# Kernel tuning notes

Measured on AMD Instinct MI355X. Metric: run time of the kernel, lower is better.

Reference implementation:

```python
import jax, jax.numpy as jnp
import numpy as np

B, N, DX, E, H, HD, KH, FF = 8, 8192, 2, 128, 8, 16, 32, 128
G1, G2, PMAX = 32, 32, 32


def _ln(x, g, b):
    mu = jnp.mean(x, axis=-1, keepdims=True)
    var = jnp.mean((x - mu) ** 2, axis=-1, keepdims=True)
    return (x - mu) * jax.lax.rsqrt(var + 1e-5) * g + b


def _cumcount_row(idx):
    # for each element, number of earlier elements with the same value (stable)
    n = idx.shape[0]
    order = jnp.argsort(idx)  # stable
    si = idx[order]
    ar = jnp.arange(n)
    is_start = jnp.concatenate([jnp.ones((1,), bool), si[1:] != si[:-1]])
    seg_start = jax.lax.associative_scan(jnp.maximum, jnp.where(is_start, ar, 0))
    return jnp.zeros(n, jnp.int32).at[order].set((ar - seg_start).astype(jnp.int32))


def _forward(x, z, latent, Wq, Wk, Wv, Wo, bo, kW1, kb1, kW2, kb2,
             lnq_g, lnq_b, lnk_g, lnk_b, ln2_g, ln2_b, fW1, fb1, fW2, fb2,
             grid_n1, grid_n2, max_patch, num_heads):
    Bb, Nn, dx = x.shape
    e = latent.shape[0]
    dims = (grid_n1, grid_n2)
    M = grid_n1 * grid_n2
    P = max_patch
    h = num_heads
    hd = Wq.shape[1] // h
    # grid range from data (margin = 0), regular grid via linspace
    mins = [jnp.min(x[:, :, i]) for i in range(dx)]
    maxs = [jnp.max(x[:, :, i]) for i in range(dx)]
    axes = [jnp.linspace(mins[i], maxs[i], dims[i]) for i in range(dx)]
    x_grid = jnp.stack(jnp.meshgrid(*axes, indexing="ij"), axis=-1)  # [G1,G2,dx]
    x_grid_flat = x_grid.reshape(M, dx)
    # nearest grid cell per point: regular grid -> per-dim rounding
    flat = None
    for i in range(dx):
        step = (maxs[i] - mins[i]) / (dims[i] - 1)
        ii = jnp.clip(jnp.round((x[..., i] - mins[i]) / step), 0, dims[i] - 1).astype(jnp.int32)
        flat = ii if flat is None else flat * dims[i] + ii
    cell = flat  # [B,N]
    cumc = jax.vmap(_cumcount_row)(cell)          # slot within cell
    slot = jnp.where(cumc < P, cumc, P)           # overflow -> dummy slot (dropped)
    bidx = jnp.broadcast_to(jnp.arange(Bb)[:, None], (Bb, Nn))
    # scatter points into per-cell padded neighbour sets [B, M, P, d]
    jx = jnp.zeros((Bb, M, P + 1, dx), x.dtype).at[bidx, cell, slot].set(x)[:, :, :P]
    jz = jnp.zeros((Bb, M, P + 1, e), z.dtype).at[bidx, cell, slot].set(z)[:, :, :P]
    msk = jnp.zeros((Bb, M, P + 1), bool).at[bidx, cell, slot].set(True)[:, :, :P]
    xg = jnp.broadcast_to(x_grid_flat[None], (Bb, M, dx))
    zg = jnp.broadcast_to(latent[None, None, :], (Bb, M, e))
    # concatenate_x_grid=True: grid token prepended, always attended
    joint_x = jnp.concatenate([xg[:, :, None, :], jx], axis=2).reshape(Bb * M, P + 1, dx)
    joint_z = jnp.concatenate([zg[:, :, None, :], jz], axis=2).reshape(Bb * M, P + 1, e)
    att_mask = jnp.concatenate([jnp.ones((Bb, M, 1), bool), msk], axis=2).reshape(Bb * M, P + 1)
    xq = xg.reshape(Bb * M, 1, dx)
    zq = zg.reshape(Bb * M, 1, e)
    T = Bb * M
    # masked translation-equivariant cross-attention (pre-norm layer)
    q = jnp.einsum("tqe,ef->tqf", _ln(zq, lnq_g, lnq_b), Wq).reshape(T, 1, h, hd)
    zk_n = _ln(joint_z, lnk_g, lnk_b)
    k = jnp.einsum("tke,ef->tkf", zk_n, Wk).reshape(T, P + 1, h, hd)
    v = jnp.einsum("tke,ef->tkf", zk_n, Wv).reshape(T, P + 1, h, hd)
    dots = jnp.einsum("tqhd,tkhd->thqk", q, k) / jnp.sqrt(jnp.asarray(hd, q.dtype))
    diff = joint_x[:, None, :, :] - xq[:, :, None, :]            # [T,1,P+1,dx]
    kb = jnp.maximum(diff @ kW1 + kb1, 0.0) @ kW2 + kb2          # kernel bias [T,1,P+1,h]
    dots = dots + jnp.transpose(kb, (0, 3, 1, 2))
    dots = jnp.where(att_mask[:, None, None, :], dots, -1e9)
    A = jax.nn.softmax(dots, axis=-1)                            # [T,h,1,P+1]
    out = jnp.einsum("thqk,tkhd->tqhd", A, v).reshape(T, 1, h * hd)
    z_new = zq + out @ Wo + bo
    z_new = z_new + (jnp.maximum(_ln(z_new, ln2_g, ln2_b) @ fW1 + fb1, 0.0) @ fW2 + fb2)
    x_new = jnp.einsum("tqk,tkd->tqd", jnp.mean(A, axis=1), joint_x)  # TE location update
    x_grid_out = x_new.reshape(Bb, grid_n1, grid_n2, dx)
    z_grid_out = z_new.reshape(Bb, grid_n1, grid_n2, e)
    return (x_grid_out, z_grid_out)


def setup_inputs():
    key = jax.random.key(0)
    ks = jax.random.split(key, 12)
    s = 0.05
    return {
        "x": jax.random.uniform(ks[0], (B, N, DX), jnp.float32),
        "z": jax.random.normal(ks[1], (B, N, E), jnp.float32),
        "grid_n1": G1, "grid_n2": G2, "max_patch": PMAX, "num_heads": H,
        "latent": jax.random.normal(ks[2], (E,), jnp.float32),
        "Wq": jax.random.normal(ks[3], (E, H * HD), jnp.float32) * s,
        "Wk": jax.random.normal(ks[4], (E, H * HD), jnp.float32) * s,
        "Wv": jax.random.normal(ks[5], (E, H * HD), jnp.float32) * s,
        "Wo": jax.random.normal(ks[6], (H * HD, E), jnp.float32) * s,
        "bo": jnp.zeros((E,), jnp.float32),
        "kW1": jax.random.normal(ks[7], (DX, KH), jnp.float32) * s,
        "kb1": jnp.zeros((KH,), jnp.float32),
        "kW2": jax.random.normal(ks[8], (KH, H), jnp.float32) * s,
        "kb2": jnp.zeros((H,), jnp.float32),
        "lnq_g": jnp.ones((E,), jnp.float32), "lnq_b": jnp.zeros((E,), jnp.float32),
        "lnk_g": jnp.ones((E,), jnp.float32), "lnk_b": jnp.zeros((E,), jnp.float32),
        "ln2_g": jnp.ones((E,), jnp.float32), "ln2_b": jnp.zeros((E,), jnp.float32),
        "fW1": jax.random.normal(ks[9], (E, FF), jnp.float32) * s,
        "fb1": jnp.zeros((FF,), jnp.float32),
        "fW2": jax.random.normal(ks[10], (FF, E), jnp.float32) * s,
        "fb2": jnp.zeros((E,), jnp.float32),
    }


def reference(x, z, grid_n1, grid_n2, max_patch, num_heads, latent, Wq, Wk, Wv, Wo, bo,
              kW1, kb1, kW2, kb2, lnq_g, lnq_b, lnk_g, lnk_b, ln2_g, ln2_b,
              fW1, fb1, fW2, fb2):
    return _forward(x, z, latent, Wq, Wk, Wv, Wo, bo, kW1, kb1, kW2, kb2,
                    lnq_g, lnq_b, lnk_g, lnk_b, ln2_g, ln2_b, fW1, fb1, fW2, fb2,
                    grid_n1, grid_n2, max_patch, num_heads)
```

## Files before the change

kernel.cpp:

```cpp
#include <hip/hip_runtime.h>
#include <stdint.h>

#define NB 8
#define NN 8192
#define NE 128
#define NH 8
#define NHD 16
#define NKH 32
#define NFF 128
#define NG 32
#define NM 1024
#define NP 32
#define NT 8192
#define NPTS 65536

typedef __attribute__((ext_vector_type(8))) short bf16x8_t;
typedef __attribute__((ext_vector_type(4))) float f32x4_t;

#define WS_MM      0
#define WS_D0      64
#define WS_Q       128
#define WS_VG      640
#define WS_PART    1152
#define WS_CNT     2048
#define WS_CELL    34816
#define WS_PIDX    296960
#define WS_WVT     1345536
#define WS_WOT     1411072
#define WS_FW1T    1443840
#define WS_FW2T    1476608
#define WS_WKQT    1509376
#define WS_SCORES  1513472
#define WS_KV      4194304

__device__ __forceinline__ unsigned short f2bf(float f) {
    unsigned u = __float_as_uint(f);
    u += 0x7FFFu + ((u >> 16) & 1u);
    return (unsigned short)(u >> 16);
}
__device__ __forceinline__ float bflo(unsigned w) { return __uint_as_float(w << 16); }
__device__ __forceinline__ float bfhi(unsigned w) { return __uint_as_float(w & 0xFFFF0000u); }

__global__ __launch_bounds__(256) void k_setup(
        const float* __restrict__ x,
        const float* __restrict__ Wk, const float* __restrict__ Wv, const float* __restrict__ Wo,
        const float* __restrict__ fW1, const float* __restrict__ fW2,
        const float* __restrict__ latent, const float* __restrict__ Wq,
        const float* __restrict__ lnq_g, const float* __restrict__ lnq_b,
        const float* __restrict__ lnk_g, const float* __restrict__ lnk_b,
        const float* __restrict__ kb1, const float* __restrict__ kW2, const float* __restrict__ kb2,
        int* __restrict__ cnt,
        unsigned short* __restrict__ WvT, unsigned short* __restrict__ WoT,
        unsigned short* __restrict__ fW1T, unsigned short* __restrict__ fW2T,
        float* __restrict__ ws_q, float* __restrict__ ws_vg, float* __restrict__ ws_d0,
        unsigned short* __restrict__ WkqT,
        float4* __restrict__ part) {
    int blk = blockIdx.x;
    int t = threadIdx.x;
    if (blk < 16) {
        __shared__ float s_t[64][65];
        const float* src; unsigned short* dst;
        int n0, k0;
        if (blk < 4) {
            int tn = blk >> 1, tk = blk & 1;
            n0 = tn * 64; k0 = tk * 64;
            src = Wv; dst = WvT;
        } else {
            int m = (blk - 4) >> 2, s4 = (blk - 4) & 3;
            int tn = s4 >> 1, tk = s4 & 1;
            n0 = tn * 64; k0 = tk * 64;
            src = (m == 0) ? Wo : (m == 1) ? fW1 : fW2;
            dst = (m == 0) ? WoT : (m == 1) ? fW1T : fW2T;
        }
        int tx = t & 63, ty = t >> 6;
        #pragma unroll
        for (int r = 0; r < 16; ++r) {
            int kr = r * 4 + ty;
            s_t[kr][tx] = src[(k0 + kr) * 128 + n0 + tx];
        }
        __syncthreads();
        #pragma unroll
        for (int r = 0; r < 16; ++r) {
            int nr = r * 4 + ty;
            dst[(n0 + nr) * 128 + k0 + tx] = f2bf(s_t[tx][nr]);
        }
    } else if (blk < 48) {
        int idx = (blk - 16) * 256 + t;
        cnt[idx] = 0;
    } else if (blk == 48) {
        __shared__ float s_qn[128], s_kn[128], s_q[128], s_kg[128];
        __shared__ float s_mu, s_rstd;
        if (t < 64) {
            float v0 = latent[t], v1 = latent[t + 64];
            float s = v0 + v1;
            for (int m = 32; m > 0; m >>= 1) s += __shfl_xor(s, m);
            float mu = s * (1.0f / 128.0f);
            float d0 = v0 - mu, d1 = v1 - mu;
            float q = d0 * d0 + d1 * d1;
            for (int m = 32; m > 0; m >>= 1) q += __shfl_xor(q, m);
            if (t == 0) { s_mu = mu; s_rstd = rsqrtf(q * (1.0f / 128.0f) + 1e-5f); }
        }
        __syncthreads();
        if (t < 128) {
            float nv = (latent[t] - s_mu) * s_rstd;
            s_qn[t] = nv * lnq_g[t] + lnq_b[t];
            s_kn[t] = nv * lnk_g[t] + lnk_b[t];
        }
        __syncthreads();
        if (t < 128) {
            float aq = 0.f, ak = 0.f, av = 0.f;
            for (int e = 0; e < 128; ++e) {
                aq += s_qn[e] * Wq[e * 128 + t];
                ak += s_kn[e] * Wk[e * 128 + t];
                av += s_kn[e] * Wv[e * 128 + t];
            }
            s_q[t] = aq; s_kg[t] = ak;
            ws_q[t] = aq; ws_vg[t] = av;
        }
        __syncthreads();
        if (t < 128) {
            const float* wr = Wk + t * 128;
            #pragma unroll
            for (int h = 0; h < 8; ++h) {
                float a = 0.f;
                #pragma unroll
                for (int d = 0; d < 16; ++d) a += wr[h * 16 + d] * s_q[h * 16 + d];
                WkqT[h * 128 + t] = f2bf(a * 0.25f);
                WkqT[(h + 8) * 128 + t] = 0;
            }
        }
        if (t < 8) {
            float acc = 0.f;
            for (int d = 0; d < 16; ++d) acc += s_q[t * 16 + d] * s_kg[t * 16 + d];
            float kb0 = kb2[t];
            for (int j = 0; j < 32; ++j) kb0 += fmaxf(kb1[j], 0.f) * kW2[j * 8 + t];
            ws_d0[t] = acc * 0.25f + kb0;
        }
    } else {
        __shared__ float s_red[4][4];
        int pb = blk - 49;
        const float4* xp = (const float4*)x + pb * 1024;
        float mn0 = 1e30f, mx0 = -1e30f, mn1 = 1e30f, mx1 = -1e30f;
        #pragma unroll
        for (int it = 0; it < 4; ++it) {
            float4 v = xp[it * 256 + t];
            mn0 = fminf(mn0, fminf(v.x, v.z)); mx0 = fmaxf(mx0, fmaxf(v.x, v.z));
            mn1 = fminf(mn1, fminf(v.y, v.w)); mx1 = fmaxf(mx1, fmaxf(v.y, v.w));
        }
        #pragma unroll
        for (int m = 32; m > 0; m >>= 1) {
            mn0 = fminf(mn0, __shfl_xor(mn0, m)); mx0 = fmaxf(mx0, __shfl_xor(mx0, m));
            mn1 = fminf(mn1, __shfl_xor(mn1, m)); mx1 = fmaxf(mx1, __shfl_xor(mx1, m));
        }
        int w = t >> 6;
        if ((t & 63) == 0) {
            s_red[w][0] = mn0; s_red[w][1] = mn1; s_red[w][2] = mx0; s_red[w][3] = mx1;
        }
        __syncthreads();
        if (t == 0) {
            float a0 = fminf(fminf(s_red[0][0], s_red[1][0]), fminf(s_red[2][0], s_red[3][0]));
            float a1 = fminf(fminf(s_red[0][1], s_red[1][1]), fminf(s_red[2][1], s_red[3][1]));
            float b0 = fmaxf(fmaxf(s_red[0][2], s_red[1][2]), fmaxf(s_red[2][2], s_red[3][2]));
            float b1 = fmaxf(fmaxf(s_red[0][3], s_red[1][3]), fmaxf(s_red[2][3], s_red[3][3]));
            part[pb] = make_float4(a0, a1, b0, b1);
        }
    }
}

__global__ __launch_bounds__(256) void k_binkv(
        const float* __restrict__ x, const float* __restrict__ z,
        const float4* __restrict__ part, float* __restrict__ mm,
        const float* __restrict__ lnk_g, const float* __restrict__ lnk_b,
        const unsigned short* __restrict__ WkqT,
        const float* __restrict__ kW1, const float* __restrict__ kb1,
        const float* __restrict__ kW2, const float* __restrict__ kb2,
        const unsigned short* __restrict__ WvT, unsigned short* __restrict__ kv,
        float* __restrict__ scores,
        int* __restrict__ cell, int* __restrict__ cnt, int* __restrict__ ptIdx) {
    int t = threadIdx.x;
    if (blockIdx.x >= 1024) {
        int l = t & 63;
        float mn0 = 1e30f, mn1 = 1e30f, mx0 = -1e30f, mx1 = -1e30f;
        if (l < 32) { float4 p = part[l]; mn0 = p.x; mn1 = p.y; mx0 = p.z; mx1 = p.w; }
        #pragma unroll
        for (int m = 32; m > 0; m >>= 1) {
            mn0 = fminf(mn0, __shfl_xor(mn0, m)); mx0 = fmaxf(mx0, __shfl_xor(mx0, m));
            mn1 = fminf(mn1, __shfl_xor(mn1, m)); mx1 = fmaxf(mx1, __shfl_xor(mx1, m));
        }
        if (blockIdx.x == 1024 && t == 0) {
            mm[0] = mn0; mm[1] = mn1; mm[2] = mx0; mm[3] = mx1;
        }
        int i = (blockIdx.x - 1024) * 256 + t;
        float st0 = (mx0 - mn0) / 31.0f, st1 = (mx1 - mn1) / 31.0f;
        float2 xv = ((const float2*)x)[i];
        int i0 = (int)rintf((xv.x - mn0) / st0); i0 = min(max(i0, 0), 31);
        int i1 = (int)rintf((xv.y - mn1) / st1); i1 = min(max(i1, 0), 31);
        int c = i0 * 32 + i1;
        cell[i] = c;
        int bb = i >> 13;
        int slot = atomicAdd(&cnt[bb * NM + c], 1);
        if (slot < NP) ptIdx[(bb * NM + c) * NP + slot] = i & (NN - 1);
        return;
    }
    __shared__ unsigned short s_zn[64][136];
    __shared__ unsigned short s_stage[4][16][68];
    int w = t >> 6, lane = t & 63;
    long base = (long)blockIdx.x * 64;
    int sub = lane >> 5;
    int lq = lane & 31;
    int mrow = lane & 15, quad = lane >> 4;

    float mn0 = 1e30f, mn1 = 1e30f, mx0 = -1e30f, mx1 = -1e30f;
    if (lane < 32) { float4 p = part[lane]; mn0 = p.x; mn1 = p.y; mx0 = p.z; mx1 = p.w; }
    #pragma unroll
    for (int m = 32; m > 0; m >>= 1) {
        mn0 = fminf(mn0, __shfl_xor(mn0, m)); mx0 = fmaxf(mx0, __shfl_xor(mx0, m));
        mn1 = fminf(mn1, __shfl_xor(mn1, m)); mx1 = fmaxf(mx1, __shfl_xor(mx1, m));
    }
    int ptl = w * 16 + mrow;
    float2 xv2 = ((const float2*)x)[base + ptl];

    int th = w >> 1, fh = w & 1;
    bf16x8_t afrag[4][4];
    #pragma unroll
    for (int j = 0; j < 4; ++j) {
        const unsigned short* ap = WvT + ((fh * 4 + j) * 16 + mrow) * 128 + quad * 8;
        #pragma unroll
        for (int kc = 0; kc < 4; ++kc)
            afrag[j][kc] = *(const bf16x8_t*)(ap + kc * 32);
    }
    bf16x8_t sfrag[4];
    #pragma unroll
    for (int kc = 0; kc < 4; ++kc)
        sfrag[kc] = *(const bf16x8_t*)(WkqT + mrow * 128 + kc * 32 + quad * 8);

    float4 g4 = ((const float4*)lnk_g)[lq];
    float4 b4 = ((const float4*)lnk_b)[lq];
    float4 v[8];
    #pragma unroll
    for (int i = 0; i < 8; ++i) {
        int pl = w * 16 + i * 2 + sub;
        v[i] = ((const float4*)z)[(base + pl) * 32 + lq];
    }
    #pragma unroll
    for (int i = 0; i < 8; ++i) {
        int pl = w * 16 + i * 2 + sub;
        float sum = v[i].x + v[i].y + v[i].z + v[i].w;
        float ssq = v[i].x * v[i].x + v[i].y * v[i].y + v[i].z * v[i].z + v[i].w * v[i].w;
        #pragma unroll
        for (int m = 1; m < 32; m <<= 1) {
            sum += __shfl_xor(sum, m);
            ssq += __shfl_xor(ssq, m);
        }
        float mu = sum * (1.0f / 128.0f);
        float var = fmaxf(ssq * (1.0f / 128.0f) - mu * mu, 0.0f);
        float rstd = rsqrtf(var + 1e-5f);
        float n0 = (v[i].x - mu) * rstd * g4.x + b4.x;
        float n1 = (v[i].y - mu) * rstd * g4.y + b4.y;
        float n2 = (v[i].z - mu) * rstd * g4.z + b4.z;
        float n3 = (v[i].w - mu) * rstd * g4.w + b4.w;
        unsigned d0 = (unsigned)f2bf(n0) | ((unsigned)f2bf(n1) << 16);
        unsigned d1 = (unsigned)f2bf(n2) | ((unsigned)f2bf(n3) << 16);
        *(uint2*)&s_zn[pl][lq * 4] = make_uint2(d0, d1);
    }
    __syncthreads();

    #pragma unroll
    for (int tau = 0; tau < 2; ++tau) {
        int trow = th * 32 + tau * 16;
        bf16x8_t bfrag[4];
        #pragma unroll
        for (int kc = 0; kc < 4; ++kc)
            bfrag[kc] = *(const bf16x8_t*)&s_zn[trow + mrow][kc * 32 + quad * 8];
        #pragma unroll
        for (int j = 0; j < 4; ++j) {
            f32x4_t acc = {0.f, 0.f, 0.f, 0.f};
            #pragma unroll
            for (int kc = 0; kc < 4; ++kc)
                acc = __builtin_amdgcn_mfma_f32_16x16x32_bf16(afrag[j][kc], bfrag[kc], acc, 0, 0, 0);
            unsigned d0 = (unsigned)f2bf(acc[0]) | ((unsigned)f2bf(acc[1]) << 16);
            unsigned d1 = (unsigned)f2bf(acc[2]) | ((unsigned)f2bf(acc[3]) << 16);
            *(uint2*)&s_stage[w][mrow][j * 16 + quad * 4] = make_uint2(d0, d1);
        }
        int tok = lane >> 3, u = lane & 7;
        long tk0 = base + trow;
        uint4 ra = *(const uint4*)&s_stage[w][tok][u * 8];
        *(uint4*)(kv + (tk0 + tok) * 128 + fh * 64 + u * 8) = ra;
        uint4 rb = *(const uint4*)&s_stage[w][tok + 8][u * 8];
        *(uint4*)(kv + (tk0 + tok + 8) * 128 + fh * 64 + u * 8) = rb;
    }

    f32x4_t sacc = {0.f, 0.f, 0.f, 0.f};
    {
        bf16x8_t sb[4];
        #pragma unroll
        for (int kc = 0; kc < 4; ++kc)
            sb[kc] = *(const bf16x8_t*)&s_zn[w * 16 + mrow][kc * 32 + quad * 8];
        #pragma unroll
        for (int kc = 0; kc < 4; ++kc)
            sacc = __builtin_amdgcn_mfma_f32_16x16x32_bf16(sfrag[kc], sb[kc], sacc, 0, 0, 0);
    }

    {
        float st0 = (mx0 - mn0) / 31.0f, st1 = (mx1 - mn1) / 31.0f;
        int i0 = (int)rintf((xv2.x - mn0) / st0); i0 = min(max(i0, 0), 31);
        int i1 = (int)rintf((xv2.y - mn1) / st1); i1 = min(max(i1, 0), 31);
        float cx0 = (i0 == 31) ? mx0 : mn0 + i0 * st0;
        float cx1 = (i1 == 31) ? mx1 : mn1 + i1 * st1;
        float d0 = xv2.x - cx0, d1 = xv2.y - cx1;
        float k0 = 0.f, k1 = 0.f, k2 = 0.f, k3 = 0.f, k4 = 0.f, k5 = 0.f, k6 = 0.f, k7 = 0.f;
        #pragma unroll
        for (int jj = 0; jj < 8; ++jj) {
            int j = quad * 8 + jj;
            float hj = fmaf(d0, kW1[j], fmaf(d1, kW1[32 + j], kb1[j]));
            hj = fmaxf(hj, 0.f);
            float4 w2a = *(const float4*)(kW2 + j * 8);
            float4 w2b = *(const float4*)(kW2 + j * 8 + 4);
            k0 = fmaf(hj, w2a.x, k0); k1 = fmaf(hj, w2a.y, k1);
            k2 = fmaf(hj, w2a.z, k2); k3 = fmaf(hj, w2a.w, k3);
            k4 = fmaf(hj, w2b.x, k4); k5 = fmaf(hj, w2b.y, k5);
            k6 = fmaf(hj, w2b.z, k6); k7 = fmaf(hj, w2b.w, k7);
        }
        k0 += __shfl_xor(k0, 16); k0 += __shfl_xor(k0, 32);
        k1 += __shfl_xor(k1, 16); k1 += __shfl_xor(k1, 32);
        k2 += __shfl_xor(k2, 16); k2 += __shfl_xor(k2, 32);
        k3 += __shfl_xor(k3, 16); k3 += __shfl_xor(k3, 32);
        k4 += __shfl_xor(k4, 16); k4 += __shfl_xor(k4, 32);
        k5 += __shfl_xor(k5, 16); k5 += __shfl_xor(k5, 32);
        k6 += __shfl_xor(k6, 16); k6 += __shfl_xor(k6, 32);
        k7 += __shfl_xor(k7, 16); k7 += __shfl_xor(k7, 32);
        if (quad == 0) {
            float4 kb2v = ((const float4*)kb2)[0];
            float4 o;
            o.x = sacc[0] + k0 + kb2v.x; o.y = sacc[1] + k1 + kb2v.y;
            o.z = sacc[2] + k2 + kb2v.z; o.w = sacc[3] + k3 + kb2v.w;
            *(float4*)(scores + ((size_t)(base + ptl)) * 8) = o;
        } else if (quad == 1) {
            float4 kb2v = ((const float4*)kb2)[1];
            float4 o;
            o.x = sacc[0] + k4 + kb2v.x; o.y = sacc[1] + k5 + kb2v.y;
            o.z = sacc[2] + k6 + kb2v.z; o.w = sacc[3] + k7 + kb2v.w;
            *(float4*)(scores + ((size_t)(base + ptl)) * 8 + 4) = o;
        }
    }
}

__global__ __launch_bounds__(256) void k_attn(const float* __restrict__ x,
        const int* __restrict__ cell, const int* __restrict__ cnt, int* __restrict__ ptIdx,
        const float* __restrict__ mm, const unsigned short* __restrict__ kv,
        const float* __restrict__ scores,
        const float* __restrict__ ws_vg, const float* __restrict__ ws_d0,
        const float* __restrict__ latent, const float* __restrict__ bo,
        const float* __restrict__ ln2_g, const float* __restrict__ ln2_b,
        const float* __restrict__ fb1, const float* __restrict__ fb2,
        const unsigned short* __restrict__ WoT, const unsigned short* __restrict__ fW1T,
        const unsigned short* __restrict__ fW2T,
        float* __restrict__ xout, float* __restrict__ zout) {
    __shared__ unsigned short s_a[16][136];
    __shared__ unsigned short s_a2[16][136];
    __shared__ float s_z[16][128];
    __shared__ float s_lat[128], s_g2[128], s_b2[128], s_fb1v[128], s_fb2v[128];
    int t = threadIdx.x;
    int l = t & 63;
    int w = t >> 6;
    int h = l >> 3, jp = l & 7;
    int base16 = blockIdx.x * 16;

    if (t < 128) {
        s_lat[t] = latent[t] + bo[t];
        s_g2[t] = ln2_g[t]; s_b2[t] = ln2_b[t];
        s_fb1v[t] = fb1[t]; s_fb2v[t] = fb2[t];
    }

    float mn0 = mm[0], mn1 = mm[1], mx0 = mm[2], mx1 = mm[3];
    float st0 = (mx0 - mn0) / 31.0f, st1 = (mx1 - mn1) / 31.0f;
    float vg0 = ws_vg[2 * l], vg1 = ws_vg[2 * l + 1];
    float ag = ws_d0[h];

    #pragma unroll
    for (int it = 0; it < 4; ++it) {
        int bm = base16 + w * 4 + it;
        int b = bm >> 10;
        int i0 = (bm & 1023) >> 5, i1 = bm & 31;
        float xg0 = (i0 == 31) ? mx0 : mn0 + i0 * st0;
        float xg1 = (i1 == 31) ? mx1 : mn1 + i1 * st1;
        int craw = cnt[bm];
        int c = min(craw, NP);
        if (craw > NP) {
            int mycell = bm & 1023;
            const int* cb = cell + b * NN;
            int run = 0;
            for (int ch = 0; ch < NN / 64 && run < NP; ++ch) {
                int n = ch * 64 + l;
                bool match = (cb[n] == mycell);
                unsigned long long mask = __ballot(match);
                if (match) {
                    int rank = run + __popcll(mask & ((1ull << l) - 1ull));
                    if (rank < NP) ptIdx[bm * NP + rank] = n;
                }
                run += __popcll(mask);
            }
        }

        int idxreg = 0; float x0r = 0.f, x1r = 0.f;
        if (l < c) {
            idxreg = ptIdx[bm * NP + l];
            float2 xv = ((const float2*)x)[(size_t)b * NN + idxreg];
            x0r = xv.x; x1r = xv.y;
        }

        float areg[4];
        areg[0] = areg[1] = areg[2] = areg[3] = -1e30f;
        #pragma unroll
        for (int g = 0; g < 4; ++g) {
            if (c > g * 8) {
                int key = g * 8 + jp;
                int idxk = __shfl(idxreg, key);
                if (key < c)
                    areg[g] = scores[((size_t)b * NN + idxk) * 8 + h];
            }
        }
        unsigned vreg[16];
        #pragma unroll
        for (int g = 0; g < 2; ++g) {
            if (c > g * 8) {
                #pragma unroll
                for (int k8 = 0; k8 < 8; ++k8) {
                    int key = g * 8 + k8;
                    if (key < c) {
                        int idxk = __shfl(idxreg, key);
                        vreg[key] = ((const unsigned*)kv)[((size_t)(b * NN + idxk) << 6) + l];
                    }
                }
            }
        }

        float mx = fmaxf(fmaxf(areg[0], areg[1]), fmaxf(areg[2], areg[3]));
        mx = fmaxf(mx, ag);
        mx = fmaxf(mx, __shfl_xor(mx, 1));
        mx = fmaxf(mx, __shfl_xor(mx, 2));
        mx = fmaxf(mx, __shfl_xor(mx, 4));
        float e0 = __expf(areg[0] - mx), e1 = __expf(areg[1] - mx);
        float e2 = __expf(areg[2] - mx), e3 = __expf(areg[3] - mx);
        float eg = __expf(ag - mx);
        float s = e0 + e1 + e2 + e3;
        s += __shfl_xor(s, 1);
        s += __shfl_xor(s, 2);
        s += __shfl_xor(s, 4);
        s += eg;
        float inv = 1.0f / s;

        float accA = eg * inv * vg0, accB = eg * inv * vg1;
        #pragma unroll
        for (int g = 0; g < 2; ++g) {
            if (c > g * 8) {
                float em = (g == 0) ? e0 : e1;
                #pragma unroll
                for (int k8 = 0; k8 < 8; ++k8) {
                    int key = g * 8 + k8;
                    if (key < c) {
                        float a = __shfl(em, (l & 56) | k8) * inv;
                        unsigned vw = vreg[key];
                        accA = fmaf(a, bflo(vw), accA);
                        accB = fmaf(a, bfhi(vw), accB);
                    }
                }
            }
        }
        #pragma unroll
        for (int g = 2; g < 4; ++g) {
            if (c > g * 8) {
                float em = (g == 2) ? e2 : e3;
                #pragma unroll
                for (int k8 = 0; k8 < 8; ++k8) {
                    int key = g * 8 + k8;
                    if (key < c) {
                        int idxk = __shfl(idxreg, key);
                        const unsigned* rowp = (const unsigned*)kv + ((size_t)(b * NN + idxk) << 6);
                        unsigned vw = rowp[l];
                        float a = __shfl(em, (l & 56) | k8) * inv;
                        accA = fmaf(a, bflo(vw), accA);
                        accB = fmaf(a, bfhi(vw), accB);
                    }
                }
            }
        }
        unsigned ow = ((unsigned)f2bf(accB) << 16) | (unsigned)f2bf(accA);
        *(unsigned*)&s_a[w * 4 + it][2 * l] = ow;

        float s0 = e0 * inv, s1 = e1 * inv, s2 = e2 * inv, s3 = e3 * inv, sg = eg * inv;
        #pragma unroll
        for (int m = 8; m <= 32; m <<= 1) {
            s0 += __shfl_xor(s0, m); s1 += __shfl_xor(s1, m);
            s2 += __shfl_xor(s2, m); s3 += __shfl_xor(s3, m);
            sg += __shfl_xor(sg, m);
        }
        float px0 = 0.f, px1 = 0.f;
        {
            float xx0, xx1;
            xx0 = __shfl(x0r, jp);      xx1 = __shfl(x1r, jp);
            px0 = fmaf(s0, xx0, px0);   px1 = fmaf(s0, xx1, px1);
            xx0 = __shfl(x0r, jp + 8);  xx1 = __shfl(x1r, jp + 8);
            px0 = fmaf(s1, xx0, px0);   px1 = fmaf(s1, xx1, px1);
            xx0 = __shfl(x0r, jp + 16); xx1 = __shfl(x1r, jp + 16);
            px0 = fmaf(s2, xx0, px0);   px1 = fmaf(s2, xx1, px1);
            xx0 = __shfl(x0r, jp + 24); xx1 = __shfl(x1r, jp + 24);
            px0 = fmaf(s3, xx0, px0);   px1 = fmaf(s3, xx1, px1);
        }
        px0 += __shfl_xor(px0, 1); px1 += __shfl_xor(px1, 1);
        px0 += __shfl_xor(px0, 2); px1 += __shfl_xor(px1, 2);
        px0 += __shfl_xor(px0, 4); px1 += __shfl_xor(px1, 4);
        if (l == 0) {
            xout[bm * 2]     = (px0 + sg * xg0) * 0.125f;
            xout[bm * 2 + 1] = (px1 + sg * xg1) * 0.125f;
        }
    }

    __syncthreads();
    int mrow = l & 15, quad = l >> 4;
    {
        bf16x8_t a[4];
        #pragma unroll
        for (int kc = 0; kc < 4; ++kc)
            a[kc] = *(const bf16x8_t*)&s_a[mrow][kc * 32 + quad * 8];
        #pragma unroll
        for (int cc = 0; cc < 2; ++cc) {
            int ct = w * 2 + cc;
            f32x4_t acc = {0.f, 0.f, 0.f, 0.f};
            const unsigned short* bp = WoT + (ct * 16 + mrow) * 128 + quad * 8;
            #pragma unroll
            for (int kc = 0; kc < 4; ++kc)
                acc = __builtin_amdgcn_mfma_f32_16x16x32_bf16(a[kc], *(const bf16x8_t*)(bp + kc * 32), acc, 0, 0, 0);
            int f = ct * 16 + mrow;
            #pragma unroll
            for (int r = 0; r < 4; ++r) {
                int row = quad * 4 + r;
                s_z[row][f] = acc[r] + s_lat[f];
            }
        }
    }
    __syncthreads();
    {
        #pragma unroll
        for (int i = 0; i < 4; ++i) {
            int row = w * 4 + i;
            float v0 = s_z[row][l], v1 = s_z[row][l + 64];
            float ssum = v0 + v1;
            #pragma unroll
            for (int m = 32; m > 0; m >>= 1) ssum += __shfl_xor(ssum, m);
            float mu = ssum * (1.0f / 128.0f);
            float d0 = v0 - mu, d1 = v1 - mu;
            float qq = d0 * d0 + d1 * d1;
            #pragma unroll
            for (int m = 32; m > 0; m >>= 1) qq += __shfl_xor(qq, m);
            float rstd = rsqrtf(qq * (1.0f / 128.0f) + 1e-5f);
            s_a2[row][l]      = f2bf(d0 * rstd * s_g2[l] + s_b2[l]);
            s_a2[row][l + 64] = f2bf(d1 * rstd * s_g2[l + 64] + s_b2[l + 64]);
        }
    }
    __syncthreads();
    {
        bf16x8_t a[4];
        #pragma unroll
        for (int kc = 0; kc < 4; ++kc)
            a[kc] = *(const bf16x8_t*)&s_a2[mrow][kc * 32 + quad * 8];
        #pragma unroll
        for (int cc = 0; cc < 2; ++cc) {
            int ct = w * 2 + cc;
            f32x4_t acc = {0.f, 0.f, 0.f, 0.f};
            const unsigned short* bp = fW1T + (ct * 16 + mrow) * 128 + quad * 8;
            #pragma unroll
            for (int kc = 0; kc < 4; ++kc)
                acc = __builtin_amdgcn_mfma_f32_16x16x32_bf16(a[kc], *(const bf16x8_t*)(bp + kc * 32), acc, 0, 0, 0);
            int f = ct * 16 + mrow;
            #pragma unroll
            for (int r = 0; r < 4; ++r) {
                int row = quad * 4 + r;
                s_a[row][f] = f2bf(fmaxf(acc[r] + s_fb1v[f], 0.f));
            }
        }
    }
    __syncthreads();
    {
        bf16x8_t a[4];
        #pragma unroll
        for (int kc = 0; kc < 4; ++kc)
            a[kc] = *(const bf16x8_t*)&s_a[mrow][kc * 32 + quad * 8];
        #pragma unroll
        for (int cc = 0; cc < 2; ++cc) {
            int ct = w * 2 + cc;
            f32x4_t acc = {0.f, 0.f, 0.f, 0.f};
            const unsigned short* bp = fW2T + (ct * 16 + mrow) * 128 + quad * 8;
            #pragma unroll
            for (int kc = 0; kc < 4; ++kc)
                acc = __builtin_amdgcn_mfma_f32_16x16x32_bf16(a[kc], *(const bf16x8_t*)(bp + kc * 32), acc, 0, 0, 0);
            int f = ct * 16 + mrow;
            #pragma unroll
            for (int r = 0; r < 4; ++r) {
                int row = quad * 4 + r;
                zout[(size_t)(base16 + row) * 128 + f] = s_z[row][f] + acc[r] + s_fb2v[f];
            }
        }
    }
}

extern "C" void kernel_launch(void* const* d_in, const int* in_sizes, int n_in,
                              void* d_out, int out_size, void* d_ws, size_t ws_size,
                              hipStream_t stream) {
    const float* x     = (const float*)d_in[0];
    const float* z     = (const float*)d_in[1];
    const float* latent= (const float*)d_in[6];
    const float* Wq    = (const float*)d_in[7];
    const float* Wk    = (const float*)d_in[8];
    const float* Wv    = (const float*)d_in[9];
    const float* Wo    = (const float*)d_in[10];
    const float* bo    = (const float*)d_in[11];
    const float* kW1   = (const float*)d_in[12];
    const float* kb1   = (const float*)d_in[13];
    const float* kW2   = (const float*)d_in[14];
    const float* kb2   = (const float*)d_in[15];
    const float* lnq_g = (const float*)d_in[16];
    const float* lnq_b = (const float*)d_in[17];
    const float* lnk_g = (const float*)d_in[18];
    const float* lnk_b = (const float*)d_in[19];
    const float* ln2_g = (const float*)d_in[20];
    const float* ln2_b = (const float*)d_in[21];
    const float* fW1   = (const float*)d_in[22];
    const float* fb1   = (const float*)d_in[23];
    const float* fW2   = (const float*)d_in[24];
    const float* fb2   = (const float*)d_in[25];

    uint8_t* ws = (uint8_t*)d_ws;
    float* mm     = (float*)(ws + WS_MM);
    float* ws_d0  = (float*)(ws + WS_D0);
    float* ws_q   = (float*)(ws + WS_Q);
    float* ws_vg  = (float*)(ws + WS_VG);
    float4* part  = (float4*)(ws + WS_PART);
    int* cnt      = (int*)(ws + WS_CNT);
    int* cell     = (int*)(ws + WS_CELL);
    int* ptIdx    = (int*)(ws + WS_PIDX);
    unsigned short* WvT  = (unsigned short*)(ws + WS_WVT);
    unsigned short* WoT  = (unsigned short*)(ws + WS_WOT);
    unsigned short* fW1T = (unsigned short*)(ws + WS_FW1T);
    unsigned short* fW2T = (unsigned short*)(ws + WS_FW2T);
    unsigned short* WkqT = (unsigned short*)(ws + WS_WKQT);
    float* scores = (float*)(ws + WS_SCORES);
    unsigned short* kv   = (unsigned short*)(ws + WS_KV);

    float* xout = (float*)d_out;
    float* zout = (float*)d_out + 16384;

    k_setup <<<81,   256, 0, stream>>>(x, Wk, Wv, Wo, fW1, fW2, latent, Wq,
                                       lnq_g, lnq_b, lnk_g, lnk_b, kb1, kW2, kb2,
                                       cnt, WvT, WoT, fW1T, fW2T, ws_q, ws_vg, ws_d0,
                                       WkqT, part);
    k_binkv <<<1280, 256, 0, stream>>>(x, z, part, mm, lnk_g, lnk_b, WkqT,
                                       kW1, kb1, kW2, kb2, WvT, kv, scores,
                                       cell, cnt, ptIdx);
    k_attn  <<<512,  256, 0, stream>>>(x, cell, cnt, ptIdx, mm, kv, scores,
                                       ws_vg, ws_d0,
                                       latent, bo, ln2_g, ln2_b, fb1, fb2,
                                       WoT, fW1T, fW2T, xout, zout);
}
```

Measured before the change: 170.9 us.

## Fuse binning into KV kernel and scatter scores/coords into cell-ordered buffers

After: 172.6 us. Within noise of the previous version (+1.0%).

```diff
diff --git a/kernel.cpp b/kernel.cpp
--- a/kernel.cpp
+++ b/kernel.cpp
@@ -26,12 +26,14 @@
 #define WS_CELL    34816
 #define WS_PIDX    296960
 #define WS_WVT     1345536
-#define WS_WOT     1411072
-#define WS_FW1T    1443840
-#define WS_FW2T    1476608
-#define WS_WKQT    1509376
-#define WS_SCORES  1513472
-#define WS_KV      4194304
+#define WS_WOT     1378304
+#define WS_FW1T    1411072
+#define WS_FW2T    1443840
+#define WS_WKQT    1476608
+#define WS_SCORES  1480704
+#define WS_XD      3577856
+#define WS_SD      5675008
+#define WS_KV      14063616
 
 __device__ __forceinline__ unsigned short f2bf(float f) {
     unsigned u = __float_as_uint(f);
@@ -175,35 +177,12 @@
         const float* __restrict__ kW1, const float* __restrict__ kb1,
         const float* __restrict__ kW2, const float* __restrict__ kb2,
         const unsigned short* __restrict__ WvT, unsigned short* __restrict__ kv,
-        float* __restrict__ scores,
+        float* __restrict__ scores, float* __restrict__ sd, float2* __restrict__ xd,
         int* __restrict__ cell, int* __restrict__ cnt, int* __restrict__ ptIdx) {
-    int t = threadIdx.x;
-    if (blockIdx.x >= 1024) {
-        int l = t & 63;
-        float mn0 = 1e30f, mn1 = 1e30f, mx0 = -1e30f, mx1 = -1e30f;
-        if (l < 32) { float4 p = part[l]; mn0 = p.x; mn1 = p.y; mx0 = p.z; mx1 = p.w; }
-        #pragma unroll
-        for (int m = 32; m > 0; m >>= 1) {
-            mn0 = fminf(mn0, __shfl_xor(mn0, m)); mx0 = fmaxf(mx0, __shfl_xor(mx0, m));
-            mn1 = fminf(mn1, __shfl_xor(mn1, m)); mx1 = fmaxf(mx1, __shfl_xor(mx1, m));
-        }
-        if (blockIdx.x == 1024 && t == 0) {
-            mm[0] = mn0; mm[1] = mn1; mm[2] = mx0; mm[3] = mx1;
-        }
-        int i = (blockIdx.x - 1024) * 256 + t;
-        float st0 = (mx0 - mn0) / 31.0f, st1 = (mx1 - mn1) / 31.0f;
-        float2 xv = ((const float2*)x)[i];
-        int i0 = (int)rintf((xv.x - mn0) / st0); i0 = min(max(i0, 0), 31);
-        int i1 = (int)rintf((xv.y - mn1) / st1); i1 = min(max(i1, 0), 31);
-        int c = i0 * 32 + i1;
-        cell[i] = c;
-        int bb = i >> 13;
-        int slot = atomicAdd(&cnt[bb * NM + c], 1);
-        if (slot < NP) ptIdx[(bb * NM + c) * NP + slot] = i & (NN - 1);
-        return;
-    }
     __shared__ unsigned short s_zn[64][136];
     __shared__ unsigned short s_stage[4][16][68];
+    __shared__ int s_dsl[64];
+    int t = threadIdx.x;
     int w = t >> 6, lane = t & 63;
     long base = (long)blockIdx.x * 64;
     int sub = lane >> 5;
@@ -216,6 +195,9 @@
     for (int m = 32; m > 0; m >>= 1) {
         mn0 = fminf(mn0, __shfl_xor(mn0, m)); mx0 = fmaxf(mx0, __shfl_xor(mx0, m));
         mn1 = fminf(mn1, __shfl_xor(mn1, m)); mx1 = fmaxf(mx1, __shfl_xor(mx1, m));
+    }
+    if (blockIdx.x == 0 && t == 0) {
+        mm[0] = mn0; mm[1] = mn1; mm[2] = mx0; mm[3] = mx1;
     }
     int ptl = w * 16 + mrow;
     float2 xv2 = ((const float2*)x)[base + ptl];
@@ -263,6 +245,20 @@
         unsigned d1 = (unsigned)f2bf(n2) | ((unsigned)f2bf(n3) << 16);
         *(uint2*)&s_zn[pl][lq * 4] = make_uint2(d0, d1);
     }
+
+    float st0 = (mx0 - mn0) / 31.0f, st1 = (mx1 - mn1) / 31.0f;
+    int i0 = (int)rintf((xv2.x - mn0) / st0); i0 = min(max(i0, 0), 31);
+    int i1 = (int)rintf((xv2.y - mn1) / st1); i1 = min(max(i1, 0), 31);
+    if (quad == 0) {
+        long gi = base + ptl;
+        int bb = (int)(gi >> 13);
+        int cellc = (bb << 10) + i0 * 32 + i1;
+        int slot = atomicAdd(&cnt[cellc], 1);
+        int ds = (slot < NP) ? ((cellc << 5) + slot) : -1;
+        s_dsl[ptl] = ds;
+        cell[gi] = i0 * 32 + i1;
+        if (ds >= 0) ptIdx[ds] = (int)(gi & (NN - 1));
+    }
     __syncthreads();
 
     #pragma unroll
@@ -302,9 +298,6 @@
     }
 
     {
-        float st0 = (mx0 - mn0) / 31.0f, st1 = (mx1 - mn1) / 31.0f;
-        int i0 = (int)rintf((xv2.x - mn0) / st0); i0 = min(max(i0, 0), 31);
-        int i1 = (int)rintf((xv2.y - mn1) / st1); i1 = min(max(i1, 0), 31);
         float cx0 = (i0 == 31) ? mx0 : mn0 + i0 * st0;
         float cx1 = (i1 == 31) ? mx1 : mn1 + i1 * st1;
         float d0 = xv2.x - cx0, d1 = xv2.y - cx1;
@@ -329,18 +322,23 @@
         k5 += __shfl_xor(k5, 16); k5 += __shfl_xor(k5, 32);
         k6 += __shfl_xor(k6, 16); k6 += __shfl_xor(k6, 32);
         k7 += __shfl_xor(k7, 16); k7 += __shfl_xor(k7, 32);
+        int dslv = s_dsl[ptl];
         if (quad == 0) {
             float4 kb2v = ((const float4*)kb2)[0];
             float4 o;
             o.x = sacc[0] + k0 + kb2v.x; o.y = sacc[1] + k1 + kb2v.y;
             o.z = sacc[2] + k2 + kb2v.z; o.w = sacc[3] + k3 + kb2v.w;
             *(float4*)(scores + ((size_t)(base + ptl)) * 8) = o;
+            if (dslv >= 0) *(float4*)(sd + (size_t)dslv * 8) = o;
         } else if (quad == 1) {
             float4 kb2v = ((const float4*)kb2)[1];
             float4 o;
             o.x = sacc[0] + k4 + kb2v.x; o.y = sacc[1] + k5 + kb2v.y;
             o.z = sacc[2] + k6 + kb2v.z; o.w = sacc[3] + k7 + kb2v.w;
             *(float4*)(scores + ((size_t)(base + ptl)) * 8 + 4) = o;
+            if (dslv >= 0) *(float4*)(sd + (size_t)dslv * 8 + 4) = o;
+        } else if (quad == 2) {
+            if (dslv >= 0) xd[dslv] = xv2;
         }
     }
 }
@@ -349,6 +347,7 @@
         const int* __restrict__ cell, const int* __restrict__ cnt, int* __restrict__ ptIdx,
         const float* __restrict__ mm, const unsigned short* __restrict__ kv,
         const float* __restrict__ scores,
+        const float* __restrict__ sd, const float2* __restrict__ xd,
         const float* __restrict__ ws_vg, const float* __restrict__ ws_d0,
         const float* __restrict__ latent, const float* __restrict__ bo,
         const float* __restrict__ ln2_g, const float* __restrict__ ln2_b,
@@ -366,6 +365,20 @@
     int h = l >> 3, jp = l & 7;
     int base16 = blockIdx.x * 16;
 
+    int craws[4]; float scvA[4][4]; float2 xvA[4][4]; int idxA[4];
+    #pragma unroll
+    for (int tt = 0; tt < 4; ++tt) {
+        int bm = base16 + w * 4 + tt;
+        size_t db = (size_t)bm << 5;
+        craws[tt] = cnt[bm];
+        #pragma unroll
+        for (int g = 0; g < 4; ++g) {
+            scvA[tt][g] = sd[(db + (size_t)(g * 8 + jp)) * 8 + h];
+            xvA[tt][g]  = xd[db + g * 8 + jp];
+        }
+        idxA[tt] = ptIdx[bm * NP + (l & (NP - 1))] & (NN - 1);
+    }
+
     if (t < 128) {
         s_lat[t] = latent[t] + bo[t];
         s_g2[t] = ln2_g[t]; s_b2[t] = ln2_b[t];
@@ -384,9 +397,23 @@
         int i0 = (bm & 1023) >> 5, i1 = bm & 31;
         float xg0 = (i0 == 31) ? mx0 : mn0 + i0 * st0;
         float xg1 = (i1 == 31) ? mx1 : mn1 + i1 * st1;
-        int craw = cnt[bm];
+        int craw = craws[it];
         int c = min(craw, NP);
-        if (craw > NP) {
+
+        int idxreg;
+        float areg[4];
+        float kx0[4], kx1[4];
+        areg[0] = areg[1] = areg[2] = areg[3] = -1e30f;
+        if (craw <= NP) {
+            idxreg = idxA[it];
+            #pragma unroll
+            for (int g = 0; g < 4; ++g) {
+                bool kvld = (g * 8 + jp < c);
+                if (kvld) areg[g] = scvA[it][g];
+                kx0[g] = kvld ? xvA[it][g].x : 0.f;
+                kx1[g] = kvld ? xvA[it][g].y : 0.f;
+            }
+        } else {
             int mycell = bm & 1023;
             const int* cb = cell + b * NN;
             int run = 0;
@@ -400,26 +427,23 @@
                 }
                 run += __popcll(mask);
             }
-        }
-
-        int idxreg = 0; float x0r = 0.f, x1r = 0.f;
-        if (l < c) {
-            idxreg = ptIdx[bm * NP + l];
-            float2 xv = ((const float2*)x)[(size_t)b * NN + idxreg];
-            x0r = xv.x; x1r = xv.y;
-        }
-
-        float areg[4];
-        areg[0] = areg[1] = areg[2] = areg[3] = -1e30f;
-        #pragma unroll
-        for (int g = 0; g < 4; ++g) {
-            if (c > g * 8) {
+            idxreg = 0; float x0r = 0.f, x1r = 0.f;
+            if (l < c) {
+                idxreg = ptIdx[bm * NP + l];
+                float2 xv = ((const float2*)x)[(size_t)b * NN + idxreg];
+                x0r = xv.x; x1r = xv.y;
+            }
+            #pragma unroll
+            for (int g = 0; g < 4; ++g) {
                 int key = g * 8 + jp;
                 int idxk = __shfl(idxreg, key);
                 if (key < c)
                     areg[g] = scores[((size_t)b * NN + idxk) * 8 + h];
-            }
-        }
+                kx0[g] = __shfl(x0r, key);
+                kx1[g] = __shfl(x1r, key);
+            }
+        }
+
         unsigned vreg[16];
         #pragma unroll
         for (int g = 0; g < 2; ++g) {
@@ -496,17 +520,10 @@
             sg += __shfl_xor(sg, m);
         }
         float px0 = 0.f, px1 = 0.f;
-        {
-            float xx0, xx1;
-            xx0 = __shfl(x0r, jp);      xx1 = __shfl(x1r, jp);
-            px0 = fmaf(s0, xx0, px0);   px1 = fmaf(s0, xx1, px1);
-            xx0 = __shfl(x0r, jp + 8);  xx1 = __shfl(x1r, jp + 8);
-            px0 = fmaf(s1, xx0, px0);   px1 = fmaf(s1, xx1, px1);
-            xx0 = __shfl(x0r, jp + 16); xx1 = __shfl(x1r, jp + 16);
-            px0 = fmaf(s2, xx0, px0);   px1 = fmaf(s2, xx1, px1);
-            xx0 = __shfl(x0r, jp + 24); xx1 = __shfl(x1r, jp + 24);
-            px0 = fmaf(s3, xx0, px0);   px1 = fmaf(s3, xx1, px1);
-        }
+        px0 = fmaf(s0, kx0[0], px0); px1 = fmaf(s0, kx1[0], px1);
+        px0 = fmaf(s1, kx0[1], px0); px1 = fmaf(s1, kx1[1], px1);
+        px0 = fmaf(s2, kx0[2], px0); px1 = fmaf(s2, kx1[2], px1);
+        px0 = fmaf(s3, kx0[3], px0); px1 = fmaf(s3, kx1[3], px1);
         px0 += __shfl_xor(px0, 1); px1 += __shfl_xor(px1, 1);
         px0 += __shfl_xor(px0, 2); px1 += __shfl_xor(px1, 2);
         px0 += __shfl_xor(px0, 4); px1 += __shfl_xor(px1, 4);
@@ -645,6 +662,8 @@
     unsigned short* fW2T = (unsigned short*)(ws + WS_FW2T);
     unsigned short* WkqT = (unsigned short*)(ws + WS_WKQT);
     float* scores = (float*)(ws + WS_SCORES);
+    float2* xd    = (float2*)(ws + WS_XD);
+    float* sd     = (float*)(ws + WS_SD);
     unsigned short* kv   = (unsigned short*)(ws + WS_KV);
 
     float* xout = (float*)d_out;
@@ -654,10 +673,10 @@
                                        lnq_g, lnq_b, lnk_g, lnk_b, kb1, kW2, kb2,
                                        cnt, WvT, WoT, fW1T, fW2T, ws_q, ws_vg, ws_d0,
                                        WkqT, part);
-    k_binkv <<<1280, 256, 0, stream>>>(x, z, part, mm, lnk_g, lnk_b, WkqT,
-                                       kW1, kb1, kW2, kb2, WvT, kv, scores,
+    k_binkv <<<1024, 256, 0, stream>>>(x, z, part, mm, lnk_g, lnk_b, WkqT,
+                                       kW1, kb1, kW2, kb2, WvT, kv, scores, sd, xd,
                                        cell, cnt, ptIdx);
-    k_attn  <<<512,  256, 0, stream>>>(x, cell, cnt, ptIdx, mm, kv, scores,
+    k_attn  <<<512,  256, 0, stream>>>(x, cell, cnt, ptIdx, mm, kv, scores, sd, xd,
                                        ws_vg, ws_d0,
                                        latent, bo, ln2_g, ln2_b, fb1, fb2,
                                        WoT, fW1T, fW2T, xout, zout);
```
